# Optimization experiments

Measured on AMD Instinct MI355X. Metric: run time of the kernel, lower is better.

The kernel has to match this reference:

```python
import jax, jax.numpy as jnp
import numpy as np

D_MODEL = 1024
D_STATE = 16
D_CONV = 4
EXPAND = 2
D_INNER = EXPAND * D_MODEL          # 2048
DT_RANK = D_MODEL // 16             # 64
BATCH, SEQ = 4, 2048


def setup_inputs() -> dict:
    key = jax.random.key(0)
    ks = jax.random.split(key, 8)
    s = lambda k, shape, sc=0.02: jax.random.normal(k, shape, jnp.float32) * sc
    x = jax.random.normal(ks[0], (BATCH, SEQ, D_MODEL), jnp.float32)
    tau = jax.random.uniform(ks[1], (BATCH, SEQ), jnp.float32) * 7200.0  # seconds
    # S4D-real init for A
    A_log = jnp.log(jnp.broadcast_to(jnp.arange(1, D_STATE + 1, dtype=jnp.float32), (D_INNER, D_STATE)))
    return dict(
        x=x, tau=tau,
        ln_g=jnp.ones((D_MODEL,), jnp.float32),
        ln_b=jnp.zeros((D_MODEL,), jnp.float32),
        in_proj_w=s(ks[2], (2 * D_INNER, D_MODEL)),
        conv_w=s(ks[3], (D_INNER, 1, D_CONV), 0.1),   # depthwise [O, I/g=1, K]
        conv_b=jnp.zeros((D_INNER,), jnp.float32),
        x_proj_w=s(ks[4], (DT_RANK + 2 * D_STATE, D_INNER)),
        dt_proj_w=s(ks[5], (D_INNER, DT_RANK), 0.1),
        dt_proj_b=jnp.full((D_INNER,), -4.6, jnp.float32),  # softplus ~ 0.01
        A_log=A_log,
        D=jnp.ones((D_INNER,), jnp.float32),
        out_proj_w=s(ks[6], (D_MODEL, D_INNER)),
        log_decay=jnp.full((D_MODEL,), -3.0, jnp.float32),
    )


def _mamba_block(x, tau, ln_g, ln_b, in_proj_w, conv_w, conv_b, x_proj_w,
                 dt_proj_w, dt_proj_b, A_log, D, out_proj_w, log_decay):
    # LayerNorm(d_model)
    mu = jnp.mean(x, axis=-1, keepdims=True)
    var = jnp.var(x, axis=-1, keepdims=True)
    xn = (x - mu) * jax.lax.rsqrt(var + 1e-5) * ln_g + ln_b

    # in_proj -> split into conv branch and gate branch, each [B, L, d_inner]
    xz = jnp.einsum('bld,ed->ble', xn, in_proj_w)
    x_in, z = jnp.split(xz, 2, axis=-1)

    # causal depthwise conv1d over time
    xc = jax.lax.conv_general_dilated(
        x_in.transpose(0, 2, 1), conv_w, (1,), [(D_CONV - 1, 0)],
        dimension_numbers=('NCH', 'OIH', 'NCH'), feature_group_count=D_INNER)
    u = jax.nn.silu(xc.transpose(0, 2, 1) + conv_b)          # [B, L, d_inner]

    # input-dependent SSM params
    x_dbl = jnp.einsum('ble,fe->blf', u, x_proj_w)
    dt, Bm, Cm = jnp.split(x_dbl, [DT_RANK, DT_RANK + D_STATE], axis=-1)
    delta = jax.nn.softplus(jnp.einsum('blr,dr->bld', dt, dt_proj_w) + dt_proj_b)
    A = -jnp.exp(A_log)                                       # [d_inner, d_state]

    # selective scan: h_t = exp(dt*A)*h + dt*u*B_t ; y_t = <h_t, C_t>
    def step(h, inp):
        d_t, B_t, C_t, u_t = inp                              # [B,d],[B,n],[B,n],[B,d]
        h = jnp.exp(d_t[..., None] * A) * h + (d_t * u_t)[..., None] * B_t[:, None, :]
        return h, jnp.einsum('bdn,bn->bd', h, C_t)

    h0 = jnp.zeros((x.shape[0], D_INNER, D_STATE), x.dtype)
    xs = (delta.transpose(1, 0, 2), Bm.transpose(1, 0, 2),
          Cm.transpose(1, 0, 2), u.transpose(1, 0, 2))
    _, ys = jax.lax.scan(step, h0, xs)
    y = ys.transpose(1, 0, 2) + u * D
    y = y * jax.nn.silu(z)
    h_out = jnp.einsum('ble,de->bld', y, out_proj_w)          # mamba output [B,L,d_model]

    # ZOH time-decay gate + residual (dropout = identity in eval)
    tau_h = jnp.maximum(tau / 3600.0, 1e-4)[..., None]
    gate = jnp.exp(-jax.nn.softplus(log_decay) * tau_h)
    return x + h_out * gate


def reference(x, tau, ln_g, ln_b, in_proj_w, conv_w, conv_b, x_proj_w,
              dt_proj_w, dt_proj_b, A_log, D, out_proj_w, log_decay):
    return _mamba_block(x, tau, ln_g, ln_b, in_proj_w, conv_w, conv_b, x_proj_w,
                        dt_proj_w, dt_proj_b, A_log, D, out_proj_w, log_decay)
```

## Files before the change

kernel.cpp:

```cpp
#include <hip/hip_runtime.h>

typedef unsigned short u16;
typedef unsigned int u32;
typedef short s16x8 __attribute__((ext_vector_type(8)));
typedef u16 u16x8 __attribute__((ext_vector_type(8)));
typedef float f32x4 __attribute__((ext_vector_type(4)));

#define TOK 8192
#define DM 1024
#define DI 2048
#define DS 16
#define DR 64
#define NCHUNK 64
#define CH 32
#define XPN 96
#define XP_SPLIT 4
#define CONV_T 16

#define SBAR() do { asm volatile("" ::: "memory"); __builtin_amdgcn_s_barrier(); asm volatile("" ::: "memory"); } while (0)
#define WAITVM(N) do { asm volatile("s_waitcnt vmcnt(" #N ")" ::: "memory"); __builtin_amdgcn_sched_barrier(0); } while (0)
#define WAITLGKM0() do { asm volatile("s_waitcnt lgkmcnt(0)" ::: "memory"); __builtin_amdgcn_sched_barrier(0); } while (0)

__device__ __forceinline__ u16 f2bf(float f) {
    u32 u = __float_as_uint(f);
    u32 r = (u + 0x7fffu + ((u >> 16) & 1u)) >> 16;
    return (u16)r;
}
__device__ __forceinline__ float bf2f(u16 h) {
    return __uint_as_float(((u32)h) << 16);
}
__device__ __forceinline__ float softplus_f(float x) {
    return (x > 15.f) ? x : __logf(1.f + __expf(x));
}
__device__ __forceinline__ void unpack8(const uint4 v, float* o) {
    o[0] = __uint_as_float(v.x << 16); o[1] = __uint_as_float(v.x & 0xffff0000u);
    o[2] = __uint_as_float(v.y << 16); o[3] = __uint_as_float(v.y & 0xffff0000u);
    o[4] = __uint_as_float(v.z << 16); o[5] = __uint_as_float(v.z & 0xffff0000u);
    o[6] = __uint_as_float(v.w << 16); o[7] = __uint_as_float(v.w & 0xffff0000u);
}
__device__ __forceinline__ void async16(u16* lds, const u16* g) {
    __builtin_amdgcn_global_load_lds(
        (const __attribute__((address_space(1))) void*)g,
        (__attribute__((address_space(3))) void*)lds, 16, 0, 0);
}

__global__ __launch_bounds__(256) void cvt_all(
    const float* __restrict__ in_w, const float* __restrict__ xp_w,
    const float* __restrict__ dt_w, const float* __restrict__ out_w,
    const float* __restrict__ tau, const float* __restrict__ log_decay,
    u16* __restrict__ wi, u16* __restrict__ wxp, u16* __restrict__ wdt,
    u16* __restrict__ wout, float* __restrict__ th, float* __restrict__ sd) {
    const int b = blockIdx.x;
    const float* src; u16* dst; int i;
    if (b < 4096)      { src = in_w;  dst = wi;   i = b * 256 + threadIdx.x; }
    else if (b < 4288) { src = xp_w;  dst = wxp;  i = (b - 4096) * 256 + threadIdx.x; }
    else if (b < 4416) { src = dt_w;  dst = wdt;  i = (b - 4288) * 256 + threadIdx.x; }
    else if (b < 6464) { src = out_w; dst = wout; i = (b - 4416) * 256 + threadIdx.x; }
    else {
        int j = (b - 6464) * 256 + threadIdx.x;
        if (j < TOK) th[j] = fmaxf(tau[j] * (1.f / 3600.f), 1e-4f);
        if (j < DM)  sd[j] = softplus_f(log_decay[j]);
        return;
    }
    float4 v = ((const float4*)src)[i];
    ushort4 o;
    o.x = f2bf(v.x); o.y = f2bf(v.y); o.z = f2bf(v.z); o.w = f2bf(v.w);
    ((ushort4*)dst)[i] = o;
}

__global__ __launch_bounds__(256) void ln_kernel(const float* __restrict__ x,
                                                 const float* __restrict__ g,
                                                 const float* __restrict__ bb,
                                                 u16* __restrict__ xn) {
    const int tok = blockIdx.x;
    const float4 v = ((const float4*)(x + (size_t)tok * DM))[threadIdx.x];
    float s = v.x + v.y + v.z + v.w;
    float sq = v.x * v.x + v.y * v.y + v.z * v.z + v.w * v.w;
#pragma unroll
    for (int off = 32; off; off >>= 1) {
        s += __shfl_xor(s, off);
        sq += __shfl_xor(sq, off);
    }
    __shared__ float red[8];
    const int wv = threadIdx.x >> 6;
    if ((threadIdx.x & 63) == 0) { red[wv] = s; red[4 + wv] = sq; }
    __syncthreads();
    s = red[0] + red[1] + red[2] + red[3];
    sq = red[4] + red[5] + red[6] + red[7];
    const float mean = s * (1.f / DM);
    const float var = sq * (1.f / DM) - mean * mean;
    const float rstd = rsqrtf(var + 1e-5f);
    const float4 gv = ((const float4*)g)[threadIdx.x];
    const float4 bv = ((const float4*)bb)[threadIdx.x];
    ushort4 o;
    o.x = f2bf((v.x - mean) * rstd * gv.x + bv.x);
    o.y = f2bf((v.y - mean) * rstd * gv.y + bv.y);
    o.z = f2bf((v.z - mean) * rstd * gv.z + bv.z);
    o.w = f2bf((v.w - mean) * rstd * gv.w + bv.w);
    ((ushort4*)(xn + (size_t)tok * DM))[threadIdx.x] = o;
}

__global__ __launch_bounds__(512) void gemm256(
    const u16* __restrict__ A, int lda,
    const u16* __restrict__ W, int ldw, int K,
    u16* __restrict__ Cxi, u16* __restrict__ Cz) {
    __shared__ __align__(16) u16 lds[2 * 32768];
    const int tid = threadIdx.x;
    const int wave = tid >> 6, lane = tid & 63;
    const int wm = wave >> 2, wn = wave & 3;
    const int fl = lane & 15, fh = lane >> 4;
    const int swz = ((int)blockIdx.x & 7) * 64 + ((int)blockIdx.x >> 3);
    const int rg = swz >> 4, wi_ = swz & 15;
    const int bm = (rg >> 2) * 4 + (wi_ >> 2);
    const int bn = (rg & 3) * 4 + (wi_ & 3);
    const int NT = K >> 6;

    const int r0 = tid >> 3;
    const int cb = ((tid & 7) ^ (r0 & 7)) << 3;
    const int rA = bm * 256 + r0;
    const int rB = bn * 256 + r0 + (r0 & ~31);

    f32x4 acc[8][4];
#pragma unroll
    for (int m = 0; m < 8; m++)
#pragma unroll
        for (int n = 0; n < 4; n++) acc[m][n] = f32x4{0.f, 0.f, 0.f, 0.f};

    auto stageA = [&](int buf, int h, int k0) {
#pragma unroll
        for (int j = 0; j < 2; j++)
            async16(lds + buf * 32768 + h * 8192 + j * 4096 + tid * 8,
                    A + (size_t)(rA + j * 128 + h * 64) * lda + k0 + cb);
    };
    auto stageB = [&](int buf, int h, int k0) {
#pragma unroll
        for (int j = 0; j < 2; j++)
            async16(lds + buf * 32768 + 16384 + h * 8192 + j * 4096 + tid * 8,
                    W + (size_t)(rB + j * 128 + h * 32) * ldw + k0 + cb);
    };
    auto rdA = [&](int buf, int mf, int kk) -> s16x8 {
        int r = wm * 64 + (mf & 3) * 16 + fl;
        int slot = ((kk << 2) | fh) ^ (fl & 7);
        return *(const s16x8*)(lds + buf * 32768 + (mf >> 2) * 8192 + r * 64 + slot * 8);
    };
    auto rdB = [&](int buf, int nh, int nf, int kk) -> s16x8 {
        int r = wn * 32 + nf * 16 + fl;
        int slot = ((kk << 2) | fh) ^ (fl & 7);
        return *(const s16x8*)(lds + buf * 32768 + 16384 + nh * 8192 + r * 64 + slot * 8);
    };

    stageA(0, 0, 0); stageA(0, 1, 0); stageB(0, 0, 0); stageB(0, 1, 0);
    stageA(1, 0, 64); stageB(1, 0, 64); stageB(1, 1, 64);
    WAITVM(6);
    SBAR();

    for (int t = 0; t < NT; ++t) {
        const int cur = t & 1, nxt = cur ^ 1;
        const int k2 = (t + 2) << 6;
        s16x8 ah[4][2], bh[4][2];
#pragma unroll
        for (int mf = 0; mf < 4; mf++) { ah[mf][0] = rdA(cur, mf, 0); ah[mf][1] = rdA(cur, mf, 1); }
#pragma unroll
        for (int nf = 0; nf < 2; nf++) {
            bh[nf][0] = rdB(cur, 0, nf, 0); bh[nf][1] = rdB(cur, 0, nf, 1);
            bh[2 + nf][0] = rdB(cur, 1, nf, 0); bh[2 + nf][1] = rdB(cur, 1, nf, 1);
        }
        if (t + 1 < NT) stageA(nxt, 1, (t + 1) << 6);
        SBAR();
        WAITLGKM0();
        __builtin_amdgcn_s_setprio(1);
#pragma unroll
        for (int kk = 0; kk < 2; kk++)
#pragma unroll
            for (int mf = 0; mf < 4; mf++)
#pragma unroll
                for (int nf = 0; nf < 4; nf++)
                    acc[mf][nf] = __builtin_amdgcn_mfma_f32_16x16x32_bf16(ah[mf][kk], bh[nf][kk], acc[mf][nf], 0, 0, 0);
        __builtin_amdgcn_s_setprio(0);
        __builtin_amdgcn_sched_barrier(0);
        SBAR();
#pragma unroll
        for (int mf = 0; mf < 4; mf++) { ah[mf][0] = rdA(cur, 4 + mf, 0); ah[mf][1] = rdA(cur, 4 + mf, 1); }
        if (t + 2 < NT) {
            stageA(cur, 0, k2); stageB(cur, 0, k2); stageB(cur, 1, k2);
            WAITVM(6);
        } else {
            WAITVM(0);
        }
        SBAR();
        WAITLGKM0();
        __builtin_amdgcn_s_setprio(1);
#pragma unroll
        for (int kk = 0; kk < 2; kk++)
#pragma unroll
            for (int mf = 0; mf < 4; mf++)
#pragma unroll
                for (int nf = 0; nf < 4; nf++)
                    acc[4 + mf][nf] = __builtin_amdgcn_mfma_f32_16x16x32_bf16(ah[mf][kk], bh[nf][kk], acc[4 + mf][nf], 0, 0, 0);
        __builtin_amdgcn_s_setprio(0);
        __builtin_amdgcn_sched_barrier(0);
        SBAR();
    }

    u16* dst = (bn < 8) ? Cxi : Cz;
    const int cbase = (bn < 8) ? bn * 256 : (bn - 8) * 256;
#pragma unroll
    for (int mf = 0; mf < 8; mf++)
#pragma unroll
        for (int j = 0; j < 4; j++) {
            int row = bm * 256 + wm * 128 + mf * 16 + fh * 4 + j;
#pragma unroll
            for (int n = 0; n < 4; n++) {
                int col = cbase + wn * 64 + n * 16 + fl;
                dst[(size_t)row * DI + col] = f2bf(acc[mf][n][j]);
            }
        }
}

__global__ __launch_bounds__(512) void gemm_out(
    const u16* __restrict__ A, int lda,
    const u16* __restrict__ W, int ldw, int K,
    float* __restrict__ Cf, int ldc,
    const float* __restrict__ xres, const float* __restrict__ th,
    const float* __restrict__ sd) {
    __shared__ __align__(16) u16 lds[2 * 24576];
    const int tid = threadIdx.x;
    const int wave = tid >> 6, lane = tid & 63;
    const int wm = wave >> 2, wn = wave & 3;
    const int fl = lane & 15, fh = lane >> 4;
    const int swz = ((int)blockIdx.x & 7) * 32 + ((int)blockIdx.x >> 3);
    const int rg = swz >> 3, w8 = swz & 7;
    const int bm = (rg >> 1) * 2 + (w8 >> 2);
    const int bn = (rg & 1) * 4 + (w8 & 3);
    const int NT = K >> 6;

    const int r0 = tid >> 3;
    const int cb = ((tid & 7) ^ (r0 & 7)) << 3;
    const int rA = bm * 256 + r0;
    const int rB = bn * 128 + r0;

    f32x4 acc[8][2];
#pragma unroll
    for (int m = 0; m < 8; m++)
#pragma unroll
        for (int n = 0; n < 2; n++) acc[m][n] = f32x4{0.f, 0.f, 0.f, 0.f};

    auto stageA = [&](int buf, int h, int k0) {
#pragma unroll
        for (int j = 0; j < 2; j++)
            async16(lds + buf * 24576 + h * 8192 + j * 4096 + tid * 8,
                    A + (size_t)(rA + j * 128 + h * 64) * lda + k0 + cb);
    };
    auto stageB = [&](int buf, int k0) {
#pragma unroll
        for (int j = 0; j < 2; j++)
            async16(lds + buf * 24576 + 16384 + j * 4096 + tid * 8,
                    W + (size_t)(rB + j * 64) * ldw + k0 + cb);
    };
    auto rdA = [&](int buf, int mf, int kk) -> s16x8 {
        int r = wm * 64 + (mf & 3) * 16 + fl;
        int slot = ((kk << 2) | fh) ^ (fl & 7);
        return *(const s16x8*)(lds + buf * 24576 + (mf >> 2) * 8192 + r * 64 + slot * 8);
    };
    auto rdB = [&](int buf, int nf, int kk) -> s16x8 {
        int r = wn * 32 + nf * 16 + fl;
        int slot = ((kk << 2) | fh) ^ (fl & 7);
        return *(const s16x8*)(lds + buf * 24576 + 16384 + r * 64 + slot * 8);
    };

    stageA(0, 0, 0); stageA(0, 1, 0); stageB(0, 0);
    stageA(1, 0, 64); stageB(1, 64);
    WAITVM(4);
    SBAR();

    for (int t = 0; t < NT; ++t) {
        const int cur = t & 1, nxt = cur ^ 1;
        const int k2 = (t + 2) << 6;
        s16x8 ah[4][2], bh[2][2];
#pragma unroll
        for (int mf = 0; mf < 4; mf++) { ah[mf][0] = rdA(cur, mf, 0); ah[mf][1] = rdA(cur, mf, 1); }
#pragma unroll
        for (int nf = 0; nf < 2; nf++) { bh[nf][0] = rdB(cur, nf, 0); bh[nf][1] = rdB(cur, nf, 1); }
        if (t + 1 < NT) stageA(nxt, 1, (t + 1) << 6);
        SBAR();
        WAITLGKM0();
        __builtin_amdgcn_s_setprio(1);
#pragma unroll
        for (int kk = 0; kk < 2; kk++)
#pragma unroll
            for (int mf = 0; mf < 4; mf++)
#pragma unroll
                for (int nf = 0; nf < 2; nf++)
                    acc[mf][nf] = __builtin_amdgcn_mfma_f32_16x16x32_bf16(ah[mf][kk], bh[nf][kk], acc[mf][nf], 0, 0, 0);
        __builtin_amdgcn_s_setprio(0);
        __builtin_amdgcn_sched_barrier(0);
        SBAR();
#pragma unroll
        for (int mf = 0; mf < 4; mf++) { ah[mf][0] = rdA(cur, 4 + mf, 0); ah[mf][1] = rdA(cur, 4 + mf, 1); }
        if (t + 2 < NT) {
            stageA(cur, 0, k2); stageB(cur, k2);
            WAITVM(4);
        } else {
            WAITVM(0);
        }
        SBAR();
        WAITLGKM0();
        __builtin_amdgcn_s_setprio(1);
#pragma unroll
        for (int kk = 0; kk < 2; kk++)
#pragma unroll
            for (int mf = 0; mf < 4; mf++)
#pragma unroll
                for (int nf = 0; nf < 2; nf++)
                    acc[4 + mf][nf] = __builtin_amdgcn_mfma_f32_16x16x32_bf16(ah[mf][kk], bh[nf][kk], acc[4 + mf][nf], 0, 0, 0);
        __builtin_amdgcn_s_setprio(0);
        __builtin_amdgcn_sched_barrier(0);
        SBAR();
    }

#pragma unroll
    for (int mf = 0; mf < 8; mf++)
#pragma unroll
        for (int j = 0; j < 4; j++) {
            int row = bm * 256 + wm * 128 + mf * 16 + fh * 4 + j;
            float t = th[row];
#pragma unroll
            for (int n = 0; n < 2; n++) {
                int col = bn * 128 + wn * 32 + n * 16 + fl;
                size_t idx = (size_t)row * ldc + col;
                Cf[idx] = xres[idx] + acc[mf][n][j] * __expf(-sd[col] * t);
            }
        }
}

__global__ __launch_bounds__(256) void gemm_bt(
    const u16* __restrict__ A, int lda,
    const u16* __restrict__ W,
    u16* __restrict__ Cb, int ldc,
    int M, int N, int K,
    const float* __restrict__ bias) {
    __shared__ u16 As[128 * 32];
    __shared__ u16 Bs[128 * 32];
    const int tid = threadIdx.x;
    const int wave = tid >> 6, lane = tid & 63;
    const int bm = blockIdx.x, bn = blockIdx.y;
    const int srow = lane >> 2, scol = (lane & 3) * 8;
    const int wr = wave >> 1, wc = wave & 1;
    const int fl = lane & 15, fh = lane >> 4;

    f32x4 acc[4][4];
#pragma unroll
    for (int m = 0; m < 4; m++)
#pragma unroll
        for (int n = 0; n < 4; n++) acc[m][n] = f32x4{0.f, 0.f, 0.f, 0.f};

    int ra[2], rb[2];
    u16* ldsA[2]; u16* ldsB[2];
#pragma unroll
    for (int i = 0; i < 2; i++) {
        int r = (wave * 2 + i) * 16 + srow;
        ra[i] = min(bm * 128 + r, M - 1);
        rb[i] = min(bn * 128 + r, N - 1);
        ldsA[i] = As + (wave * 2 + i) * 512 + lane * 8;
        ldsB[i] = Bs + (wave * 2 + i) * 512 + lane * 8;
    }

    for (int k0 = 0; k0 < K; k0 += 32) {
        __syncthreads();
#pragma unroll
        for (int i = 0; i < 2; i++) {
            async16(ldsA[i], A + (size_t)ra[i] * lda + k0 + scol);
            async16(ldsB[i], W + (size_t)rb[i] * K + k0 + scol);
        }
        __syncthreads();
        s16x8 av[4], bv[4];
#pragma unroll
        for (int m = 0; m < 4; m++)
            av[m] = *(const s16x8*)(As + (wr * 64 + m * 16 + fl) * 32 + fh * 8);
#pragma unroll
        for (int n = 0; n < 4; n++)
            bv[n] = *(const s16x8*)(Bs + (wc * 64 + n * 16 + fl) * 32 + fh * 8);
#pragma unroll
        for (int m = 0; m < 4; m++)
#pragma unroll
            for (int n = 0; n < 4; n++)
                acc[m][n] = __builtin_amdgcn_mfma_f32_16x16x32_bf16(av[m], bv[n], acc[m][n], 0, 0, 0);
    }

#pragma unroll
    for (int m = 0; m < 4; m++) {
#pragma unroll
        for (int j = 0; j < 4; j++) {
            int row = bm * 128 + wr * 64 + m * 16 + fh * 4 + j;
            if (row >= M) continue;
#pragma unroll
            for (int n = 0; n < 4; n++) {
                int col = bn * 128 + wc * 64 + n * 16 + fl;
                if (col >= N) continue;
                Cb[(size_t)row * ldc + col] = f2bf(softplus_f(acc[m][n][j] + bias[col]));
            }
        }
    }
}

__global__ __launch_bounds__(256) void xp_gemm(const u16* __restrict__ A,
                                               const u16* __restrict__ W,
                                               float* __restrict__ part) {
    __shared__ u16 As[128 * 64];
    __shared__ u16 Bs[XPN * 64];
    const int tid = threadIdx.x;
    const int wave = tid >> 6, lane = tid & 63;
    const int bm = blockIdx.x, sp = blockIdx.y;
    const int fl = lane & 15, fh = lane >> 4;
    const int trow = tid >> 3, tcol = (tid & 7) * 8;

    f32x4 acc[2][6];
#pragma unroll
    for (int m = 0; m < 2; m++)
#pragma unroll
        for (int n = 0; n < 6; n++) acc[m][n] = f32x4{0.f, 0.f, 0.f, 0.f};

    const int kbeg = sp * (DI / XP_SPLIT);
    for (int k0 = kbeg; k0 < kbeg + DI / XP_SPLIT; k0 += 64) {
        __syncthreads();
#pragma unroll
        for (int i = 0; i < 4; i++)
            async16(As + i * 2048 + tid * 8,
                    A + (size_t)(bm * 128 + i * 32 + trow) * DI + k0 + tcol);
#pragma unroll
        for (int i = 0; i < 3; i++)
            async16(Bs + i * 2048 + tid * 8,
                    W + (size_t)(i * 32 + trow) * DI + k0 + tcol);
        __syncthreads();
#pragma unroll
        for (int kk = 0; kk < 2; kk++) {
            s16x8 av[2], bv[6];
#pragma unroll
            for (int m = 0; m < 2; m++)
                av[m] = *(const s16x8*)(As + (wave * 32 + m * 16 + fl) * 64 + kk * 32 + fh * 8);
#pragma unroll
            for (int n = 0; n < 6; n++)
                bv[n] = *(const s16x8*)(Bs + (n * 16 + fl) * 64 + kk * 32 + fh * 8);
#pragma unroll
            for (int m = 0; m < 2; m++)
#pragma unroll
                for (int n = 0; n < 6; n++)
                    acc[m][n] = __builtin_amdgcn_mfma_f32_16x16x32_bf16(av[m], bv[n], acc[m][n], 0, 0, 0);
        }
    }
    float* dst = part + (size_t)sp * TOK * XPN;
#pragma unroll
    for (int m = 0; m < 2; m++)
#pragma unroll
        for (int j = 0; j < 4; j++) {
            int row = bm * 128 + wave * 32 + m * 16 + fh * 4 + j;
#pragma unroll
            for (int n = 0; n < 6; n++) {
                int col = n * 16 + fl;
                dst[(size_t)row * XPN + col] = acc[m][n][j];
            }
        }
}

__global__ __launch_bounds__(256) void xp_reduce(const float* __restrict__ part,
                                                 u16* __restrict__ out) {
    int i = blockIdx.x * 256 + threadIdx.x;
    if (i >= TOK * XPN) return;
    float s = 0.f;
#pragma unroll
    for (int sp = 0; sp < XP_SPLIT; sp++) s += part[(size_t)sp * TOK * XPN + i];
    out[i] = f2bf(s);
}

__global__ __launch_bounds__(256) void conv_silu_kernel(const u16* __restrict__ xi,
                                                        const float* __restrict__ cw,
                                                        const float* __restrict__ cb,
                                                        u16* __restrict__ u) {
    const int b = blockIdx.y;
    const int l0 = blockIdx.x * CONV_T;
    const int d0 = threadIdx.x * 8;
    float w0[8], w1[8], w2[8], w3[8], bias[8];
#pragma unroll
    for (int e = 0; e < 8; e++) {
        float4 wv = ((const float4*)cw)[d0 + e];
        w0[e] = wv.x; w1[e] = wv.y; w2[e] = wv.z; w3[e] = wv.w;
        bias[e] = cb[d0 + e];
    }
    float win[4][8];
#pragma unroll
    for (int i = 0; i < 3; i++) {
        int l = l0 - 3 + i;
        int slot = (l0 + 1 + i) & 3;
        if (l < 0) {
#pragma unroll
            for (int e = 0; e < 8; e++) win[slot][e] = 0.f;
        } else {
            u16x8 v = *(const u16x8*)(xi + ((size_t)(b * 2048 + l)) * DI + d0);
#pragma unroll
            for (int e = 0; e < 8; e++) win[slot][e] = bf2f(v[e]);
        }
    }
#pragma unroll
    for (int t = 0; t < CONV_T; t++) {
        const int l = l0 + t;
        const size_t tok = (size_t)b * 2048 + l;
        u16x8 v = *(const u16x8*)(xi + tok * DI + d0);
        const int s3 = t & 3;
#pragma unroll
        for (int e = 0; e < 8; e++) win[s3][e] = bf2f(v[e]);
        const int s0 = (t + 1) & 3, s1 = (t + 2) & 3, s2 = (t + 3) & 3;
        u16x8 o;
#pragma unroll
        for (int e = 0; e < 8; e++) {
            float a = bias[e];
            a = fmaf(w0[e], win[s0][e], a);
            a = fmaf(w1[e], win[s1][e], a);
            a = fmaf(w2[e], win[s2][e], a);
            a = fmaf(w3[e], win[s3][e], a);
            o[e] = f2bf(a / (1.f + __expf(-a)));
        }
        *(u16x8*)(u + tok * DI + d0) = o;
    }
}

__global__ __launch_bounds__(256) void scan_passA(const u16* __restrict__ delta,
                                                  const u16* __restrict__ u,
                                                  const u16* __restrict__ xdbl,
                                                  const float* __restrict__ A_log,
                                                  float* __restrict__ qh,
                                                  float* __restrict__ Sarr) {
    const int d = blockIdx.x * 256 + threadIdx.x;
    const int b = blockIdx.y, c = blockIdx.z;
    float Av[16];
#pragma unroll
    for (int n = 0; n < 16; n++) Av[n] = -__expf(A_log[d * 16 + n]);
    bool fast = true;
#pragma unroll
    for (int n = 0; n < 16; n++) fast = fast && (fabsf(Av[n] + (float)(n + 1)) < 1e-4f * (n + 1));
    const bool allfast = __all(fast);

    float h[16];
#pragma unroll
    for (int n = 0; n < 16; n++) h[n] = 0.f;
    float S = 0.f;
    const int l0 = c * CH;
    size_t tok = (size_t)b * 2048 + l0;
    float dt = bf2f(delta[tok * DI + d]);
    float uu = bf2f(u[tok * DI + d]);
    const uint4* bp0 = (const uint4*)(xdbl + tok * 96 + 64);
    uint4 b0 = bp0[0], b1 = bp0[1];
    for (int t = 0; t < CH; ++t) {
        const int tn = (t + 1 < CH) ? t + 1 : t;
        const size_t tokn = (size_t)b * 2048 + l0 + tn;
        float dt_n = bf2f(delta[tokn * DI + d]);
        float uu_n = bf2f(u[tokn * DI + d]);
        const uint4* bpn = (const uint4*)(xdbl + tokn * 96 + 64);
        uint4 b0n = bpn[0], b1n = bpn[1];
        float du = dt * uu;
        float Bv[16];
        unpack8(b0, Bv); unpack8(b1, Bv + 8);
        float e[16];
        if (allfast) {
            float r = __expf(-dt);
            e[0] = r;
#pragma unroll
            for (int n = 1; n < 16; n++) e[n] = e[n - 1] * r;
        } else {
#pragma unroll
            for (int n = 0; n < 16; n++) e[n] = __expf(dt * Av[n]);
        }
#pragma unroll
        for (int n = 0; n < 16; n++) h[n] = fmaf(e[n], h[n], du * Bv[n]);
        S += dt;
        dt = dt_n; uu = uu_n; b0 = b0n; b1 = b1n;
    }
    const size_t base = ((size_t)(c * 4 + b) * 16) * DI + d;
#pragma unroll
    for (int n = 0; n < 16; n++) qh[base + (size_t)n * DI] = h[n];
    Sarr[(size_t)(c * 4 + b) * DI + d] = S;
}

__global__ __launch_bounds__(256) void scan_passB(float* __restrict__ qh,
                                                  const float* __restrict__ Sarr,
                                                  const float* __restrict__ A_log) {
    const int idx = blockIdx.x * 256 + threadIdx.x;
    const int d = idx & (DI - 1);
    const int n = (idx >> 11) & 15;
    const int b = idx >> 15;
    const float Avn = -__expf(A_log[d * 16 + n]);
    float h = 0.f;
    for (int c = 0; c < NCHUNK; c++) {
        const size_t base = ((size_t)(c * 4 + b) * 16 + n) * DI + d;
        const float qv = qh[base];
        const float S = Sarr[(size_t)(c * 4 + b) * DI + d];
        qh[base] = h;
        h = fmaf(__expf(Avn * S), h, qv);
    }
}

__global__ __launch_bounds__(256) void scan_passC(const u16* __restrict__ delta,
                                                  const u16* __restrict__ u,
                                                  const u16* __restrict__ xdbl,
                                                  const u16* __restrict__ z,
                                                  const float* __restrict__ A_log,
                                                  const float* __restrict__ Dvec,
                                                  const float* __restrict__ qh,
                                                  u16* __restrict__ yg) {
    const int d = blockIdx.x * 256 + threadIdx.x;
    const int b = blockIdx.y, c = blockIdx.z;
    float Av[16];
#pragma unroll
    for (int n = 0; n < 16; n++) Av[n] = -__expf(A_log[d * 16 + n]);
    bool fast = true;
#pragma unroll
    for (int n = 0; n < 16; n++) fast = fast && (fabsf(Av[n] + (float)(n + 1)) < 1e-4f * (n + 1));
    const bool allfast = __all(fast);
    const float Dd = Dvec[d];

    float h[16];
    const size_t hbase = ((size_t)(c * 4 + b) * 16) * DI + d;
#pragma unroll
    for (int n = 0; n < 16; n++) h[n] = qh[hbase + (size_t)n * DI];

    const int l0 = c * CH;
    size_t tok = (size_t)b * 2048 + l0;
    float dt = bf2f(delta[tok * DI + d]);
    float uu = bf2f(u[tok * DI + d]);
    float zz = bf2f(z[tok * DI + d]);
    const uint4* bp0 = (const uint4*)(xdbl + tok * 96 + 64);
    uint4 b0 = bp0[0], b1 = bp0[1], c0 = bp0[2], c1 = bp0[3];
    for (int t = 0; t < CH; ++t) {
        const int tn = (t + 1 < CH) ? t + 1 : t;
        const size_t tokn = (size_t)b * 2048 + l0 + tn;
        float dt_n = bf2f(delta[tokn * DI + d]);
        float uu_n = bf2f(u[tokn * DI + d]);
        float zz_n = bf2f(z[tokn * DI + d]);
        const uint4* bpn = (const uint4*)(xdbl + tokn * 96 + 64);
        uint4 b0n = bpn[0], b1n = bpn[1], c0n = bpn[2], c1n = bpn[3];

        float du = dt * uu;
        float Bv[16], Cv[16];
        unpack8(b0, Bv); unpack8(b1, Bv + 8);
        unpack8(c0, Cv); unpack8(c1, Cv + 8);
        float e[16];
        if (allfast) {
            float r = __expf(-dt);
            e[0] = r;
#pragma unroll
            for (int n = 1; n < 16; n++) e[n] = e[n - 1] * r;
        } else {
#pragma unroll
            for (int n = 0; n < 16; n++) e[n] = __expf(dt * Av[n]);
        }
        float y = 0.f;
#pragma unroll
        for (int n = 0; n < 16; n++) {
            h[n] = fmaf(e[n], h[n], du * Bv[n]);
            y = fmaf(h[n], Cv[n], y);
        }
        float sz = zz / (1.f + __expf(-zz));
        const size_t tokc = (size_t)b * 2048 + l0 + t;
        yg[tokc * DI + d] = f2bf((y + uu * Dd) * sz);

        dt = dt_n; uu = uu_n; zz = zz_n;
        b0 = b0n; b1 = b1n; c0 = c0n; c1 = c1n;
    }
}

extern "C" void kernel_launch(void* const* d_in, const int* in_sizes, int n_in,
                              void* d_out, int out_size, void* d_ws, size_t ws_size,
                              hipStream_t stream) {
    const float* x = (const float*)d_in[0];
    const float* tau = (const float*)d_in[1];
    const float* ln_g = (const float*)d_in[2];
    const float* ln_b = (const float*)d_in[3];
    const float* in_proj_w = (const float*)d_in[4];
    const float* conv_w = (const float*)d_in[5];
    const float* conv_b = (const float*)d_in[6];
    const float* x_proj_w = (const float*)d_in[7];
    const float* dt_proj_w = (const float*)d_in[8];
    const float* dt_proj_b = (const float*)d_in[9];
    const float* A_log = (const float*)d_in[10];
    const float* Dvec = (const float*)d_in[11];
    const float* out_proj_w = (const float*)d_in[12];
    const float* log_decay = (const float*)d_in[13];
    float* out = (float*)d_out;

    char* ws = (char*)d_ws;
    size_t off = 0;
    auto alloc = [&](size_t bytes) -> void* {
        void* p = ws + off;
        off += (bytes + 255) & ~(size_t)255;
        return p;
    };
    u16* xn    = (u16*)alloc((size_t)TOK * DM * 2);
    u16* w_in  = (u16*)alloc((size_t)2 * DI * DM * 2);
    u16* w_xp  = (u16*)alloc((size_t)XPN * DI * 2);
    u16* w_dt  = (u16*)alloc((size_t)DI * DR * 2);
    u16* w_out = (u16*)alloc((size_t)DM * DI * 2);
    u16* xi    = (u16*)alloc((size_t)TOK * DI * 2);
    u16* z     = (u16*)alloc((size_t)TOK * DI * 2);
    u16* u     = (u16*)alloc((size_t)TOK * DI * 2);
    u16* xdbl  = (u16*)alloc((size_t)TOK * XPN * 2);
    u16* delta = (u16*)alloc((size_t)TOK * DI * 2);
    float* qh   = (float*)alloc((size_t)NCHUNK * 4 * 16 * DI * 4);
    float* Sarr = (float*)alloc((size_t)NCHUNK * 4 * DI * 4);
    u16* yg    = (u16*)alloc((size_t)TOK * DI * 2);
    float* th = (float*)alloc((size_t)TOK * 4);
    float* sd = (float*)alloc((size_t)DM * 4);
    float* xp_part = (float*)xn;

    cvt_all<<<6496, 256, 0, stream>>>(in_proj_w, x_proj_w, dt_proj_w, out_proj_w,
                                      tau, log_decay, w_in, w_xp, w_dt, w_out, th, sd);

    ln_kernel<<<TOK, 256, 0, stream>>>(x, ln_g, ln_b, xn);

    gemm256<<<512, 512, 0, stream>>>(xn, DM, w_in, DM, DM, xi, z);
    conv_silu_kernel<<<dim3(2048 / CONV_T, 4), 256, 0, stream>>>(xi, conv_w, conv_b, u);

    xp_gemm<<<dim3(64, XP_SPLIT), 256, 0, stream>>>(u, w_xp, xp_part);
    xp_reduce<<<(TOK * XPN + 255) / 256, 256, 0, stream>>>(xp_part, xdbl);

    gemm_bt<<<dim3(64, 16), 256, 0, stream>>>(xdbl, XPN, w_dt, delta, DI,
                                              TOK, DI, DR, dt_proj_b);

    scan_passA<<<dim3(8, 4, NCHUNK), 256, 0, stream>>>(delta, u, xdbl, A_log, qh, Sarr);
    scan_passB<<<512, 256, 0, stream>>>(qh, Sarr, A_log);
    scan_passC<<<dim3(8, 4, NCHUNK), 256, 0, stream>>>(delta, u, xdbl, z, A_log, Dvec, qh, yg);

    gemm_out<<<256, 512, 0, stream>>>(yg, DI, w_out, DI, DI, out, DM, x, th, sd);
}
```

Before: 304.3 us.

## Replace 256-tile GEMMs with templated 128x128 GEMM using two blocks per CU

Both the in_proj GEMM and the output GEMM move from large 256-row tiles with 512 threads to a single templated 128x128-tile kernel with 256 threads and launch_bounds(256,2), so two blocks can share a CU. The pipeline is simplified to one full-tile stage per double-buffered iteration, and the epilogue is chosen by a template parameter. This raises the block count (2048 and 512) for better load balance across CUs and more concurrent blocks, at the cost of less operand reuse per tile and more global/LDS traffic per FLOP.

```diff
diff --git a/kernel.cpp b/kernel.cpp
--- a/kernel.cpp
+++ b/kernel.cpp
@@ -100,74 +100,80 @@
     ((ushort4*)(xn + (size_t)tok * DM))[threadIdx.x] = o;
 }
 
-__global__ __launch_bounds__(512) void gemm256(
+template <int EPI>
+__global__ __launch_bounds__(256, 2) void gemm128(
     const u16* __restrict__ A, int lda,
     const u16* __restrict__ W, int ldw, int K,
-    u16* __restrict__ Cxi, u16* __restrict__ Cz) {
-    __shared__ __align__(16) u16 lds[2 * 32768];
+    u16* __restrict__ Cxi, u16* __restrict__ Cz,
+    float* __restrict__ Cf,
+    const float* __restrict__ xres, const float* __restrict__ th,
+    const float* __restrict__ sd) {
+    __shared__ __align__(16) u16 lds[2 * 16384];
     const int tid = threadIdx.x;
     const int wave = tid >> 6, lane = tid & 63;
-    const int wm = wave >> 2, wn = wave & 3;
+    const int wm = wave >> 1, wn = wave & 1;
     const int fl = lane & 15, fh = lane >> 4;
-    const int swz = ((int)blockIdx.x & 7) * 64 + ((int)blockIdx.x >> 3);
-    const int rg = swz >> 4, wi_ = swz & 15;
-    const int bm = (rg >> 2) * 4 + (wi_ >> 2);
-    const int bn = (rg & 3) * 4 + (wi_ & 3);
+    int bm, bn;
+    if (EPI == 0) {
+        const int swz = ((int)blockIdx.x & 7) * 256 + ((int)blockIdx.x >> 3);
+        const int rg = swz >> 5, wi_ = swz & 31;
+        bm = (rg >> 2) * 4 + (wi_ >> 3);
+        bn = (rg & 3) * 8 + (wi_ & 7);
+    } else {
+        const int swz = ((int)blockIdx.x & 7) * 64 + ((int)blockIdx.x >> 3);
+        const int rg = swz >> 4, wi_ = swz & 15;
+        bm = (rg >> 1) * 4 + (wi_ >> 2);
+        bn = (rg & 1) * 4 + (wi_ & 3);
+    }
     const int NT = K >> 6;
 
     const int r0 = tid >> 3;
     const int cb = ((tid & 7) ^ (r0 & 7)) << 3;
-    const int rA = bm * 256 + r0;
-    const int rB = bn * 256 + r0 + (r0 & ~31);
-
-    f32x4 acc[8][4];
-#pragma unroll
-    for (int m = 0; m < 8; m++)
+    const int rA = bm * 128 + r0;
+    const int rB = bn * 128 + r0;
+
+    f32x4 acc[4][4];
+#pragma unroll
+    for (int m = 0; m < 4; m++)
 #pragma unroll
         for (int n = 0; n < 4; n++) acc[m][n] = f32x4{0.f, 0.f, 0.f, 0.f};
 
-    auto stageA = [&](int buf, int h, int k0) {
-#pragma unroll
-        for (int j = 0; j < 2; j++)
-            async16(lds + buf * 32768 + h * 8192 + j * 4096 + tid * 8,
-                    A + (size_t)(rA + j * 128 + h * 64) * lda + k0 + cb);
-    };
-    auto stageB = [&](int buf, int h, int k0) {
-#pragma unroll
-        for (int j = 0; j < 2; j++)
-            async16(lds + buf * 32768 + 16384 + h * 8192 + j * 4096 + tid * 8,
-                    W + (size_t)(rB + j * 128 + h * 32) * ldw + k0 + cb);
+    auto stage = [&](int buf, int k0) {
+#pragma unroll
+        for (int j = 0; j < 4; j++)
+            async16(lds + buf * 16384 + j * 2048 + tid * 8,
+                    A + (size_t)(rA + j * 32) * lda + k0 + cb);
+#pragma unroll
+        for (int j = 0; j < 4; j++)
+            async16(lds + buf * 16384 + 8192 + j * 2048 + tid * 8,
+                    W + (size_t)(rB + j * 32) * ldw + k0 + cb);
     };
     auto rdA = [&](int buf, int mf, int kk) -> s16x8 {
-        int r = wm * 64 + (mf & 3) * 16 + fl;
+        int r = wm * 64 + mf * 16 + fl;
         int slot = ((kk << 2) | fh) ^ (fl & 7);
-        return *(const s16x8*)(lds + buf * 32768 + (mf >> 2) * 8192 + r * 64 + slot * 8);
+        return *(const s16x8*)(lds + buf * 16384 + r * 64 + slot * 8);
     };
-    auto rdB = [&](int buf, int nh, int nf, int kk) -> s16x8 {
-        int r = wn * 32 + nf * 16 + fl;
+    auto rdB = [&](int buf, int nf, int kk) -> s16x8 {
+        int r = wn * 64 + nf * 16 + fl;
         int slot = ((kk << 2) | fh) ^ (fl & 7);
-        return *(const s16x8*)(lds + buf * 32768 + 16384 + nh * 8192 + r * 64 + slot * 8);
+        return *(const s16x8*)(lds + buf * 16384 + 8192 + r * 64 + slot * 8);
     };
 
-    stageA(0, 0, 0); stageA(0, 1, 0); stageB(0, 0, 0); stageB(0, 1, 0);
-    stageA(1, 0, 64); stageB(1, 0, 64); stageB(1, 1, 64);
-    WAITVM(6);
+    stage(0, 0);
+    stage(1, 64);
+    WAITVM(8);
     SBAR();
 
     for (int t = 0; t < NT; ++t) {
-        const int cur = t & 1, nxt = cur ^ 1;
-        const int k2 = (t + 2) << 6;
+        const int cur = t & 1;
         s16x8 ah[4][2], bh[4][2];
 #pragma unroll
         for (int mf = 0; mf < 4; mf++) { ah[mf][0] = rdA(cur, mf, 0); ah[mf][1] = rdA(cur, mf, 1); }
 #pragma unroll
-        for (int nf = 0; nf < 2; nf++) {
-            bh[nf][0] = rdB(cur, 0, nf, 0); bh[nf][1] = rdB(cur, 0, nf, 1);
-            bh[2 + nf][0] = rdB(cur, 1, nf, 0); bh[2 + nf][1] = rdB(cur, 1, nf, 1);
-        }
-        if (t + 1 < NT) stageA(nxt, 1, (t + 1) << 6);
+        for (int nf = 0; nf < 4; nf++) { bh[nf][0] = rdB(cur, nf, 0); bh[nf][1] = rdB(cur, nf, 1); }
+        WAITLGKM0();
         SBAR();
-        WAITLGKM0();
+        if (t + 2 < NT) stage(cur, (t + 2) << 6);
         __builtin_amdgcn_s_setprio(1);
 #pragma unroll
         for (int kk = 0; kk < 2; kk++)
@@ -178,157 +184,32 @@
                     acc[mf][nf] = __builtin_amdgcn_mfma_f32_16x16x32_bf16(ah[mf][kk], bh[nf][kk], acc[mf][nf], 0, 0, 0);
         __builtin_amdgcn_s_setprio(0);
         __builtin_amdgcn_sched_barrier(0);
+        if (t + 2 < NT) { WAITVM(8); }
+        else           { WAITVM(0); }
         SBAR();
-#pragma unroll
-        for (int mf = 0; mf < 4; mf++) { ah[mf][0] = rdA(cur, 4 + mf, 0); ah[mf][1] = rdA(cur, 4 + mf, 1); }
-        if (t + 2 < NT) {
-            stageA(cur, 0, k2); stageB(cur, 0, k2); stageB(cur, 1, k2);
-            WAITVM(6);
-        } else {
-            WAITVM(0);
-        }
-        SBAR();
-        WAITLGKM0();
-        __builtin_amdgcn_s_setprio(1);
-#pragma unroll
-        for (int kk = 0; kk < 2; kk++)
-#pragma unroll
-            for (int mf = 0; mf < 4; mf++)
-#pragma unroll
-                for (int nf = 0; nf < 4; nf++)
-                    acc[4 + mf][nf] = __builtin_amdgcn_mfma_f32_16x16x32_bf16(ah[mf][kk], bh[nf][kk], acc[4 + mf][nf], 0, 0, 0);
-        __builtin_amdgcn_s_setprio(0);
-        __builtin_amdgcn_sched_barrier(0);
-        SBAR();
-    }
-
-    u16* dst = (bn < 8) ? Cxi : Cz;
-    const int cbase = (bn < 8) ? bn * 256 : (bn - 8) * 256;
-#pragma unroll
-    for (int mf = 0; mf < 8; mf++)
+    }
+
+#pragma unroll
+    for (int mf = 0; mf < 4; mf++)
 #pragma unroll
         for (int j = 0; j < 4; j++) {
-            int row = bm * 256 + wm * 128 + mf * 16 + fh * 4 + j;
-#pragma unroll
-            for (int n = 0; n < 4; n++) {
-                int col = cbase + wn * 64 + n * 16 + fl;
-                dst[(size_t)row * DI + col] = f2bf(acc[mf][n][j]);
-            }
-        }
-}
-
-__global__ __launch_bounds__(512) void gemm_out(
-    const u16* __restrict__ A, int lda,
-    const u16* __restrict__ W, int ldw, int K,
-    float* __restrict__ Cf, int ldc,
-    const float* __restrict__ xres, const float* __restrict__ th,
-    const float* __restrict__ sd) {
-    __shared__ __align__(16) u16 lds[2 * 24576];
-    const int tid = threadIdx.x;
-    const int wave = tid >> 6, lane = tid & 63;
-    const int wm = wave >> 2, wn = wave & 3;
-    const int fl = lane & 15, fh = lane >> 4;
-    const int swz = ((int)blockIdx.x & 7) * 32 + ((int)blockIdx.x >> 3);
-    const int rg = swz >> 3, w8 = swz & 7;
-    const int bm = (rg >> 1) * 2 + (w8 >> 2);
-    const int bn = (rg & 1) * 4 + (w8 & 3);
-    const int NT = K >> 6;
-
-    const int r0 = tid >> 3;
-    const int cb = ((tid & 7) ^ (r0 & 7)) << 3;
-    const int rA = bm * 256 + r0;
-    const int rB = bn * 128 + r0;
-
-    f32x4 acc[8][2];
-#pragma unroll
-    for (int m = 0; m < 8; m++)
-#pragma unroll
-        for (int n = 0; n < 2; n++) acc[m][n] = f32x4{0.f, 0.f, 0.f, 0.f};
-
-    auto stageA = [&](int buf, int h, int k0) {
-#pragma unroll
-        for (int j = 0; j < 2; j++)
-            async16(lds + buf * 24576 + h * 8192 + j * 4096 + tid * 8,
-                    A + (size_t)(rA + j * 128 + h * 64) * lda + k0 + cb);
-    };
-    auto stageB = [&](int buf, int k0) {
-#pragma unroll
-        for (int j = 0; j < 2; j++)
-            async16(lds + buf * 24576 + 16384 + j * 4096 + tid * 8,
-                    W + (size_t)(rB + j * 64) * ldw + k0 + cb);
-    };
-    auto rdA = [&](int buf, int mf, int kk) -> s16x8 {
-        int r = wm * 64 + (mf & 3) * 16 + fl;
-        int slot = ((kk << 2) | fh) ^ (fl & 7);
-        return *(const s16x8*)(lds + buf * 24576 + (mf >> 2) * 8192 + r * 64 + slot * 8);
-    };
-    auto rdB = [&](int buf, int nf, int kk) -> s16x8 {
-        int r = wn * 32 + nf * 16 + fl;
-        int slot = ((kk << 2) | fh) ^ (fl & 7);
-        return *(const s16x8*)(lds + buf * 24576 + 16384 + r * 64 + slot * 8);
-    };
-
-    stageA(0, 0, 0); stageA(0, 1, 0); stageB(0, 0);
-    stageA(1, 0, 64); stageB(1, 64);
-    WAITVM(4);
-    SBAR();
-
-    for (int t = 0; t < NT; ++t) {
-        const int cur = t & 1, nxt = cur ^ 1;
-        const int k2 = (t + 2) << 6;
-        s16x8 ah[4][2], bh[2][2];
-#pragma unroll
-        for (int mf = 0; mf < 4; mf++) { ah[mf][0] = rdA(cur, mf, 0); ah[mf][1] = rdA(cur, mf, 1); }
-#pragma unroll
-        for (int nf = 0; nf < 2; nf++) { bh[nf][0] = rdB(cur, nf, 0); bh[nf][1] = rdB(cur, nf, 1); }
-        if (t + 1 < NT) stageA(nxt, 1, (t + 1) << 6);
-        SBAR();
-        WAITLGKM0();
-        __builtin_amdgcn_s_setprio(1);
-#pragma unroll
-        for (int kk = 0; kk < 2; kk++)
-#pragma unroll
-            for (int mf = 0; mf < 4; mf++)
-#pragma unroll
-                for (int nf = 0; nf < 2; nf++)
-                    acc[mf][nf] = __builtin_amdgcn_mfma_f32_16x16x32_bf16(ah[mf][kk], bh[nf][kk], acc[mf][nf], 0, 0, 0);
-        __builtin_amdgcn_s_setprio(0);
-        __builtin_amdgcn_sched_barrier(0);
-        SBAR();
-#pragma unroll
-        for (int mf = 0; mf < 4; mf++) { ah[mf][0] = rdA(cur, 4 + mf, 0); ah[mf][1] = rdA(cur, 4 + mf, 1); }
-        if (t + 2 < NT) {
-            stageA(cur, 0, k2); stageB(cur, k2);
-            WAITVM(4);
-        } else {
-            WAITVM(0);
-        }
-        SBAR();
-        WAITLGKM0();
-        __builtin_amdgcn_s_setprio(1);
-#pragma unroll
-        for (int kk = 0; kk < 2; kk++)
-#pragma unroll
-            for (int mf = 0; mf < 4; mf++)
-#pragma unroll
-                for (int nf = 0; nf < 2; nf++)
-                    acc[4 + mf][nf] = __builtin_amdgcn_mfma_f32_16x16x32_bf16(ah[mf][kk], bh[nf][kk], acc[4 + mf][nf], 0, 0, 0);
-        __builtin_amdgcn_s_setprio(0);
-        __builtin_amdgcn_sched_barrier(0);
-        SBAR();
-    }
-
-#pragma unroll
-    for (int mf = 0; mf < 8; mf++)
-#pragma unroll
-        for (int j = 0; j < 4; j++) {
-            int row = bm * 256 + wm * 128 + mf * 16 + fh * 4 + j;
-            float t = th[row];
-#pragma unroll
-            for (int n = 0; n < 2; n++) {
-                int col = bn * 128 + wn * 32 + n * 16 + fl;
-                size_t idx = (size_t)row * ldc + col;
-                Cf[idx] = xres[idx] + acc[mf][n][j] * __expf(-sd[col] * t);
+            int row = bm * 128 + wm * 64 + mf * 16 + fh * 4 + j;
+            if (EPI == 0) {
+                u16* dst = (bn < 16) ? Cxi : Cz;
+                const int cbase = (bn < 16) ? bn * 128 : (bn - 16) * 128;
+#pragma unroll
+                for (int n = 0; n < 4; n++) {
+                    int col = cbase + wn * 64 + n * 16 + fl;
+                    dst[(size_t)row * DI + col] = f2bf(acc[mf][n][j]);
+                }
+            } else {
+                float t = th[row];
+#pragma unroll
+                for (int n = 0; n < 4; n++) {
+                    int col = bn * 128 + wn * 64 + n * 16 + fl;
+                    size_t idx = (size_t)row * DM + col;
+                    Cf[idx] = xres[idx] + acc[mf][n][j] * __expf(-sd[col] * t);
+                }
             }
         }
 }
@@ -715,7 +596,8 @@
 
     ln_kernel<<<TOK, 256, 0, stream>>>(x, ln_g, ln_b, xn);
 
-    gemm256<<<512, 512, 0, stream>>>(xn, DM, w_in, DM, DM, xi, z);
+    gemm128<0><<<2048, 256, 0, stream>>>(xn, DM, w_in, DM, DM, xi, z,
+                                         nullptr, nullptr, nullptr, nullptr);
     conv_silu_kernel<<<dim3(2048 / CONV_T, 4), 256, 0, stream>>>(xi, conv_w, conv_b, u);
 
     xp_gemm<<<dim3(64, XP_SPLIT), 256, 0, stream>>>(u, w_xp, xp_part);
@@ -728,5 +610,6 @@
     scan_passB<<<512, 256, 0, stream>>>(qh, Sarr, A_log);
     scan_passC<<<dim3(8, 4, NCHUNK), 256, 0, stream>>>(delta, u, xdbl, z, A_log, Dvec, qh, yg);
 
-    gemm_out<<<256, 512, 0, stream>>>(yg, DI, w_out, DI, DI, out, DM, x, th, sd);
-}
+    gemm128<2><<<512, 256, 0, stream>>>(yg, DI, w_out, DI, DI, nullptr, nullptr,
+                                        out, x, th, sd);
+}
```

Result: no change. 307.5 us (+1.0%).
